# Performance work log

Hardware: AMD Instinct MI355X
Metric: run time of the kernel (lower is better)

## Reference

```python
import jax, jax.numpy as jnp
import numpy as np

CHUNK = 2048   # chunk_size from __init__
EPS = 1e-5     # BatchNorm eps (torch default)


def _proj(x, w, gamma, beta, mean, var):
    # 1x1 conv (no bias) + BatchNorm (eval, running stats) + ReLU
    y = jnp.einsum('bchw,oc->bohw', x, w)
    scale = gamma / jnp.sqrt(var + EPS)
    y = (y - mean[None, :, None, None]) * scale[None, :, None, None] + beta[None, :, None, None]
    return jax.nn.relu(y)


def setup_inputs() -> dict:
    key = jax.random.key(0)
    ks = jax.random.split(key, 8)
    B, Cl, Ci, Co, H, W = 2, 256, 512, 128, 128, 128
    return {
        'lidar_features': jax.random.normal(ks[0], (B, Cl, H, W), jnp.float32),
        'image_features': jax.random.normal(ks[1], (B, Ci, H, W), jnp.float32),
        # kaiming_normal fan_out for 1x1 conv: std = sqrt(2 / Co)
        'lidar_w': jax.random.normal(ks[2], (Co, Cl), jnp.float32) * np.sqrt(2.0 / Co),
        'lidar_gamma': jnp.ones((Co,), jnp.float32),
        'lidar_beta': jnp.zeros((Co,), jnp.float32),
        'lidar_mean': jax.random.normal(ks[3], (Co,), jnp.float32) * 0.1,
        'lidar_var': jax.random.uniform(ks[4], (Co,), jnp.float32, 0.5, 1.5),
        'image_w': jax.random.normal(ks[5], (Co, Ci), jnp.float32) * np.sqrt(2.0 / Co),
        'image_gamma': jnp.ones((Co,), jnp.float32),
        'image_beta': jnp.zeros((Co,), jnp.float32),
        'image_mean': jax.random.normal(ks[6], (Co,), jnp.float32) * 0.1,
        'image_var': jax.random.uniform(ks[7], (Co,), jnp.float32, 0.5, 1.5),
        'modality_weights': jnp.ones((2,), jnp.float32),
    }


def reference(lidar_features, image_features,
              lidar_w, lidar_gamma, lidar_beta, lidar_mean, lidar_var,
              image_w, image_gamma, image_beta, image_mean, image_var,
              modality_weights):
    lidar_proj = _proj(lidar_features, lidar_w, lidar_gamma, lidar_beta, lidar_mean, lidar_var)
    image_proj = _proj(image_features, image_w, image_gamma, image_beta, image_mean, image_var)
    # spatial sizes match by construction, so no interpolation branch
    B, C, H, W = lidar_proj.shape
    P = H * W
    n = P // CHUNK  # P chosen divisible by CHUNK
    # block-diagonal attention: q from image, k=v from lidar, per pixel chunk
    q = image_proj.reshape(B, C, P).transpose(0, 2, 1).reshape(B, n, CHUNK, C)
    k = lidar_proj.reshape(B, C, P).transpose(0, 2, 1).reshape(B, n, CHUNK, C)
    attn = jax.nn.softmax(jnp.einsum('bnqc,bnkc->bnqk', q, k) / jnp.sqrt(jnp.float32(C)), axis=-1)
    out = jnp.einsum('bnqk,bnkc->bnqc', attn, k)  # v == k (both are lidar_proj)
    fused = out.reshape(B, P, C).transpose(0, 2, 1).reshape(B, C, H, W)
    w = jax.nn.softmax(modality_weights)
    return w[0] * image_proj + w[1] * fused
```

## Files before the change

### kernel.cpp

```cpp
#include <hip/hip_runtime.h>
#include <hip/hip_bf16.h>

typedef __attribute__((ext_vector_type(4))) float f32x4;
typedef __attribute__((ext_vector_type(8))) short short8;

#define P_TOT 16384
#define NCO 128
#define EPS 1e-5f
#define ALPHA 0.12752269f

__device__ __forceinline__ unsigned short f2bf(float f) {
  union { float f; unsigned u; } v; v.f = f;
  unsigned r = v.u + 0x7FFFu + ((v.u >> 16) & 1u);
  return (unsigned short)(r >> 16);
}
__device__ __forceinline__ float bf2f(unsigned short h) {
  union { unsigned u; float f; } v; v.u = ((unsigned)h) << 16;
  return v.f;
}
__device__ __forceinline__ unsigned cvtpk_bf16(float lo, float hi) {
  unsigned r;
  asm("v_cvt_pk_bf16_f32 %0, %1, %2" : "=v"(r) : "v"(lo), "v"(hi));
  return r;
}
__device__ __forceinline__ void gload16(const void* g, void* l) {
  __builtin_amdgcn_global_load_lds(
      (const __attribute__((address_space(1))) unsigned*)g,
      (__attribute__((address_space(3))) unsigned*)l, 16, 0, 0);
}

__global__ __launch_bounds__(256) void proj_mfma(
    const float* __restrict__ Xl, const float* __restrict__ Xi,
    const float* __restrict__ Wl, const float* __restrict__ Wi,
    const float* __restrict__ lgm, const float* __restrict__ lbt,
    const float* __restrict__ lmn, const float* __restrict__ lvr,
    const float* __restrict__ igm, const float* __restrict__ ibt,
    const float* __restrict__ imn, const float* __restrict__ ivr,
    unsigned short* __restrict__ Lp, unsigned short* __restrict__ Ip,
    unsigned short* __restrict__ Vg)
{
  __shared__ __align__(16) char smem[36352];
  float* sc_l = (float*)(smem + 35328);
  float* sh_l = (float*)(smem + 35840);

  const int t = threadIdx.x;
  const int w = t >> 6, l = t & 63, l15 = l & 15, g = l >> 4;
  const int zz = blockIdx.y, b = zz & 1, mod = zz >> 1;
  const int pb = blockIdx.x * 128;

  const float* Xg = mod ? Xi : Xl;
  const float* Wg = mod ? Wi : Wl;
  const int Cin = mod ? 512 : 256;
  unsigned short* outp = mod ? Ip : Lp;

  if (t < 128) {
    const float* G = mod ? igm : lgm;
    const float* Bt = mod ? ibt : lbt;
    const float* M = mod ? imn : lmn;
    const float* V = mod ? ivr : lvr;
    float s = G[t] / sqrtf(V[t] + EPS);
    sc_l[t] = s;
    sh_l[t] = Bt[t] - M[t] * s;
  }

  f32x4 o[2][8];
#pragma unroll
  for (int qt = 0; qt < 2; ++qt)
#pragma unroll
    for (int nt = 0; nt < 8; ++nt) o[qt][nt] = (f32x4){0.f, 0.f, 0.f, 0.f};

  uint2 xr[8], wr[8];
  auto load_tiles = [&](int s) {
    int cc = s * 64;
#pragma unroll
    for (int i = 0; i < 8; ++i) {
      int e = t + 256 * i;
      int c = e >> 5, p4 = e & 31;
      f32x4 x = *(const f32x4*)(Xg + ((size_t)(b * Cin + cc + c)) * P_TOT + pb + p4 * 4);
      xr[i].x = cvtpk_bf16(x[0], x[1]);
      xr[i].y = cvtpk_bf16(x[2], x[3]);
    }
#pragma unroll
    for (int i = 0; i < 8; ++i) {
      int e = t + 256 * i;
      int co = e >> 4, c4 = e & 15;
      f32x4 wv = *(const f32x4*)(Wg + (size_t)co * Cin + cc + c4 * 4);
      wr[i].x = cvtpk_bf16(wv[0], wv[1]);
      wr[i].y = cvtpk_bf16(wv[2], wv[3]);
    }
  };

  load_tiles(0);
  const int nsteps = Cin >> 6;
  for (int s = 0; s < nsteps; ++s) {
    __syncthreads();
#pragma unroll
    for (int i = 0; i < 8; ++i) {
      int e = t + 256 * i;
      int c = e >> 5, p4 = e & 31;
      *(uint2*)(smem + c * 264 + p4 * 8) = xr[i];
    }
#pragma unroll
    for (int i = 0; i < 8; ++i) {
      int e = t + 256 * i;
      int co = e >> 4, c4 = e & 15;
      *(uint2*)(smem + 16896 + co * 144 + c4 * 8) = wr[i];
    }
    if (s + 1 < nsteps) load_tiles(s + 1);
    __syncthreads();

#pragma unroll
    for (int kkc = 0; kkc < 2; ++kkc) {
      short8 a[2];
#pragma unroll
      for (int qt = 0; qt < 2; ++qt) {
        const char* ab = smem + (kkc * 32 + g * 8) * 264 + (w * 32 + qt * 16 + l15) * 2;
        union { unsigned uu[4]; short8 v; } cv;
#pragma unroll
        for (int e2 = 0; e2 < 4; ++e2) {
          unsigned lo = *(const unsigned short*)(ab + (2 * e2) * 264);
          unsigned hi = *(const unsigned short*)(ab + (2 * e2 + 1) * 264);
          cv.uu[e2] = lo | (hi << 16);
        }
        a[qt] = cv.v;
      }
#pragma unroll
      for (int nt = 0; nt < 8; ++nt) {
        short8 wf = *(const short8*)(smem + 16896 + (nt * 16 + l15) * 144 + kkc * 64 + g * 16);
        o[0][nt] = __builtin_amdgcn_mfma_f32_16x16x32_bf16(a[0], wf, o[0][nt], 0, 0, 0);
        o[1][nt] = __builtin_amdgcn_mfma_f32_16x16x32_bf16(a[1], wf, o[1][nt], 0, 0, 0);
      }
    }
  }

  __syncthreads();
#pragma unroll
  for (int nt = 0; nt < 8; ++nt) {
    float scv = sc_l[nt * 16 + l15];
    float shv = sh_l[nt * 16 + l15];
#pragma unroll
    for (int qt = 0; qt < 2; ++qt)
#pragma unroll
      for (int r = 0; r < 4; ++r) {
        int p = w * 32 + qt * 16 + 4 * g + r;
        float y = fmaxf(fmaf(o[qt][nt][r], scv, shv), 0.f);
        *(unsigned short*)(smem + p * 272 + (nt * 16 + l15) * 2) = f2bf(y);
      }
  }
  __syncthreads();
  {
    int p = t >> 1, half = t & 1;
    const char* Tb = smem + p * 272 + half * 128;
    unsigned short* ob = outp + ((size_t)b * P_TOT + pb + p) * NCO + half * 64;
#pragma unroll
    for (int i = 0; i < 8; ++i)
      *(uint4*)(ob + i * 8) = *(const uint4*)(Tb + i * 16);
  }
  if (mod == 0) {
    int co = t & 127, ph = t >> 7;
    unsigned short* vb = Vg + ((size_t)b * NCO + co) * P_TOT + pb + ph * 64;
    unsigned pkv[32];
#pragma unroll
    for (int j2 = 0; j2 < 32; ++j2) {
      unsigned lo = *(const unsigned short*)(smem + (ph * 64 + 2 * j2) * 272 + co * 2);
      unsigned hi = *(const unsigned short*)(smem + (ph * 64 + 2 * j2 + 1) * 272 + co * 2);
      pkv[j2] = lo | (hi << 16);
    }
#pragma unroll
    for (int i = 0; i < 8; ++i)
      *(uint4*)(vb + i * 8) = *(const uint4*)&pkv[i * 4];
  }
}

__global__ __launch_bounds__(512) void attn_kernel(
    const unsigned short* __restrict__ Lp,
    const unsigned short* __restrict__ Ip,
    const unsigned short* __restrict__ Vg,
    const float* __restrict__ mw,
    float* __restrict__ out)
{
  __shared__ __align__(16) char smem[131072];

  const int t = threadIdx.x;
  const int half = t >> 8;
  const int t2 = t & 255;
  const int w = t2 >> 6, l = t & 63;
  const int l15 = l & 15, g = l >> 4;
  const int hb = half << 16;
  const int gid = blockIdx.x;
  const int bx = gid >> 4;
  const int chunk = gid & 7;
  const int b = (gid >> 3) & 1;
  const int pq0 = chunk * 2048 + bx * 128;
  const int qw = pq0 + w * 32;

  short8 qf[2][4];
#pragma unroll
  for (int qt = 0; qt < 2; ++qt)
#pragma unroll
    for (int kkc = 0; kkc < 4; ++kkc)
      qf[qt][kkc] = *(const short8*)(Ip +
          ((size_t)b * P_TOT + qw + qt * 16 + l15) * NCO + kkc * 32 + g * 8);

  const char* srcK[4];
  const char* srcV[4];
  int ldsOff[4];
#pragma unroll
  for (int i = 0; i < 4; ++i) {
    int pos = (w * 4 + i) * 4 + (l >> 4);
    int nt = pos >> 4, gp = (pos >> 2) & 3, rr = pos & 3;
    int kp = (nt >> 1) * 32 + gp * 8 + (nt & 1) * 4 + rr;
    srcK[i] = (const char*)Lp +
              ((size_t)b * P_TOT + chunk * 2048 + half * 1024 + kp) * 256 +
              (((l & 15) * 16) ^ ((pos & 7) << 4));
    int c = (w * 4 + i) * 8 + (l >> 3);
    srcV[i] = (const char*)Vg +
              (((size_t)(b * NCO + c)) * P_TOT + chunk * 2048 + half * 1024) * 2 +
              (((l & 7) * 16) ^ ((c & 7) << 4));
    ldsOff[i] = hb + (w * 4 + i) * 1024;
  }

  float m_[2] = {-1e30f, -1e30f}, lsum[2] = {0.f, 0.f};
  f32x4 o[2][8];
#pragma unroll
  for (int qt = 0; qt < 2; ++qt)
#pragma unroll
    for (int ct = 0; ct < 8; ++ct) o[qt][ct] = (f32x4){0.f, 0.f, 0.f, 0.f};

#pragma unroll
  for (int i = 0; i < 4; ++i) {
    gload16(srcK[i], smem + ldsOff[i]);
    gload16(srcV[i], smem + 32768 + ldsOff[i]);
  }
#pragma unroll
  for (int i = 0; i < 4; ++i) {
    gload16(srcK[i] + 16384, smem + 16384 + ldsOff[i]);
    gload16(srcV[i] + 128, smem + 32768 + 16384 + ldsOff[i]);
  }

  for (int kt = 0; kt < 16; ++kt) {
    const int cur = kt & 1;
    if (kt < 15)
      asm volatile("s_waitcnt vmcnt(8)" ::: "memory");
    else
      asm volatile("s_waitcnt vmcnt(0)" ::: "memory");
    __builtin_amdgcn_s_barrier();
    __builtin_amdgcn_sched_barrier(0);

    const char* Kb = smem + hb + cur * 16384;
    const char* Vb = smem + hb + 32768 + cur * 16384;

    f32x4 s[2][4];
#pragma unroll
    for (int qt = 0; qt < 2; ++qt)
#pragma unroll
      for (int nt = 0; nt < 4; ++nt) s[qt][nt] = (f32x4){0.f, 0.f, 0.f, 0.f};
#pragma unroll
    for (int kkc = 0; kkc < 4; ++kkc) {
#pragma unroll
      for (int nt = 0; nt < 4; ++nt) {
        short8 kf = *(const short8*)(Kb + (nt * 16 + l15) * 256 +
                        ((kkc * 64 + g * 16) ^ ((l15 & 7) << 4)));
        s[0][nt] = __builtin_amdgcn_mfma_f32_16x16x32_bf16(kf, qf[0][kkc], s[0][nt], 0, 0, 0);
        s[1][nt] = __builtin_amdgcn_mfma_f32_16x16x32_bf16(kf, qf[1][kkc], s[1][nt], 0, 0, 0);
      }
    }

    unsigned pk[2][4][2];
    float f_[2];
    int upd[2];
#pragma unroll
    for (int qt = 0; qt < 2; ++qt) {
      float v0 = fmaxf(fmaxf(s[qt][0][0], s[qt][0][1]), fmaxf(s[qt][0][2], s[qt][0][3]));
      float v1 = fmaxf(fmaxf(s[qt][1][0], s[qt][1][1]), fmaxf(s[qt][1][2], s[qt][1][3]));
      float v2 = fmaxf(fmaxf(s[qt][2][0], s[qt][2][1]), fmaxf(s[qt][2][2], s[qt][2][3]));
      float v3 = fmaxf(fmaxf(s[qt][3][0], s[qt][3][1]), fmaxf(s[qt][3][2], s[qt][3][3]));
      float v = fmaxf(fmaxf(v0, v1), fmaxf(v2, v3));
      v = fmaxf(v, __shfl_xor(v, 16));
      v = fmaxf(v, __shfl_xor(v, 32));
      float pm = v * ALPHA;
      upd[qt] = __any(pm > m_[qt] + 8.f);
      float mn = m_[qt];
      if (upd[qt]) {
        mn = fmaxf(m_[qt], pm);
        f_[qt] = __builtin_amdgcn_exp2f(m_[qt] - mn);
        m_[qt] = mn;
      } else {
        f_[qt] = 1.f;
      }
      float ps = 0.f;
#pragma unroll
      for (int nt = 0; nt < 4; ++nt) {
#pragma unroll
        for (int r = 0; r < 4; ++r) {
          float p = __builtin_amdgcn_exp2f(s[qt][nt][r] * ALPHA - mn);
          s[qt][nt][r] = p;
          ps += p;
        }
        pk[qt][nt][0] = cvtpk_bf16(s[qt][nt][0], s[qt][nt][1]);
        pk[qt][nt][1] = cvtpk_bf16(s[qt][nt][2], s[qt][nt][3]);
      }
      ps += __shfl_xor(ps, 16);
      ps += __shfl_xor(ps, 32);
      lsum[qt] = lsum[qt] * f_[qt] + ps;
    }

#pragma unroll
    for (int qt = 0; qt < 2; ++qt)
      if (upd[qt]) {
#pragma unroll
        for (int r = 0; r < 4; ++r) {
          float fb = __shfl(f_[qt], 20 * g + r);
#pragma unroll
          for (int ct = 0; ct < 8; ++ct) o[qt][ct][r] *= fb;
        }
      }

#pragma unroll
    for (int kk2 = 0; kk2 < 2; ++kk2) {
      short8 af[2];
#pragma unroll
      for (int qt = 0; qt < 2; ++qt) {
        union { unsigned u[4]; short8 v; } x;
        x.u[0] = pk[qt][2 * kk2][0];
        x.u[1] = pk[qt][2 * kk2][1];
        x.u[2] = pk[qt][2 * kk2 + 1][0];
        x.u[3] = pk[qt][2 * kk2 + 1][1];
        af[qt] = x.v;
      }
#pragma unroll
      for (int ct = 0; ct < 8; ++ct) {
        short8 vf = *(const short8*)(Vb + (ct * 16 + l15) * 128 +
                        ((kk2 * 64 + g * 16) ^ ((l15 & 7) << 4)));
        o[0][ct] = __builtin_amdgcn_mfma_f32_16x16x32_bf16(af[0], vf, o[0][ct], 0, 0, 0);
        o[1][ct] = __builtin_amdgcn_mfma_f32_16x16x32_bf16(af[1], vf, o[1][ct], 0, 0, 0);
      }
    }

    __builtin_amdgcn_s_barrier();
    __builtin_amdgcn_sched_barrier(0);
    if (kt + 2 < 16) {
#pragma unroll
      for (int i = 0; i < 4; ++i) {
        gload16(srcK[i] + (size_t)(kt + 2) * 16384,
                smem + cur * 16384 + ldsOff[i]);
        gload16(srcV[i] + (size_t)(kt + 2) * 128,
                smem + 32768 + cur * 16384 + ldsOff[i]);
      }
    }
  }

  float* Tp = (float*)smem;
  float* m1a = (float*)(smem + 67584);
  float* l1a = (float*)(smem + 68096);

  if (half == 1) {
#pragma unroll
    for (int qt = 0; qt < 2; ++qt) {
      int qb = w * 32 + qt * 16 + 4 * g;
#pragma unroll
      for (int ct = 0; ct < 8; ++ct) {
        int c = ct * 16 + l15;
        *(f32x4*)&Tp[c * 132 + qb] = o[qt][ct];
      }
      if (g == 0) {
        m1a[w * 32 + qt * 16 + l15] = m_[qt];
        l1a[w * 32 + qt * 16 + l15] = lsum[qt];
      }
    }
  }
  __syncthreads();

  float a0 = mw[0], a1 = mw[1];
  float mx = fmaxf(a0, a1);
  float e0 = __builtin_amdgcn_exp2f((a0 - mx) * 1.442695041f);
  float e1 = __builtin_amdgcn_exp2f((a1 - mx) * 1.442695041f);
  float w0m = e0 / (e0 + e1), w1m = e1 / (e0 + e1);

  if (half == 0) {
#pragma unroll
    for (int qt = 0; qt < 2; ++qt) {
      int qb = w * 32 + qt * 16 + 4 * g;
      f32x4 m1v = *(const f32x4*)&m1a[qb];
      f32x4 l1v = *(const f32x4*)&l1a[qb];
      float A[4], Bc[4];
#pragma unroll
      for (int r = 0; r < 4; ++r) {
        float m0r = __shfl(m_[qt], 20 * g + r);
        float l0r = __shfl(lsum[qt], 20 * g + r);
        float M = fmaxf(m0r, m1v[r]);
        float w0h = __builtin_amdgcn_exp2f(m0r - M);
        float w1h = __builtin_amdgcn_exp2f(m1v[r] - M);
        float L = w0h * l0r + w1h * l1v[r];
        A[r] = w1m * w0h / L;
        Bc[r] = w1m * w1h / L;
      }
#pragma unroll
      for (int ct = 0; ct < 8; ++ct) {
        int c = ct * 16 + l15;
        f32x4 o1 = *(const f32x4*)&Tp[c * 132 + qb];
#pragma unroll
        for (int r = 0; r < 4; ++r)
          o[qt][ct][r] = A[r] * o[qt][ct][r] + Bc[r] * o1[r];
      }
    }
  }
  __syncthreads();

  if (half == 0) {
#pragma unroll
    for (int qt = 0; qt < 2; ++qt) {
      int qb = w * 32 + qt * 16 + 4 * g;
#pragma unroll
      for (int ct = 0; ct < 8; ++ct) {
        int c = ct * 16 + l15;
        f32x4 v = o[qt][ct];
#pragma unroll
        for (int r = 0; r < 4; ++r) {
          float img = bf2f(Ip[((size_t)b * P_TOT + pq0 + qb + r) * NCO + c]);
          v[r] = w0m * img + v[r];
        }
        *(f32x4*)&Tp[c * 132 + qb] = v;
      }
    }
  }
  __syncthreads();
  {
    int cc = t >> 5;
    int q0 = (t & 31) * 4;
#pragma unroll
    for (int i2 = 0; i2 < 8; ++i2) {
      int c = cc + i2 * 16;
      float* Ob = out + ((size_t)b * NCO + c) * P_TOT + pq0 + q0;
      *(f32x4*)Ob = *(const f32x4*)&Tp[c * 132 + q0];
    }
  }
}

extern "C" void kernel_launch(void* const* d_in, const int* in_sizes, int n_in,
                              void* d_out, int out_size, void* d_ws, size_t ws_size,
                              hipStream_t stream) {
  const float* lidar = (const float*)d_in[0];
  const float* image = (const float*)d_in[1];
  const float* lw = (const float*)d_in[2];
  const float* lg = (const float*)d_in[3];
  const float* lb = (const float*)d_in[4];
  const float* lm = (const float*)d_in[5];
  const float* lv = (const float*)d_in[6];
  const float* iw = (const float*)d_in[7];
  const float* ig = (const float*)d_in[8];
  const float* ibt = (const float*)d_in[9];
  const float* im = (const float*)d_in[10];
  const float* iv = (const float*)d_in[11];
  const float* mw = (const float*)d_in[12];

  unsigned short* Lp = (unsigned short*)d_ws;
  unsigned short* Ip = Lp + (size_t)2 * P_TOT * NCO;
  unsigned short* Vg = Ip + (size_t)2 * P_TOT * NCO;

  dim3 gp(P_TOT / 128, 4);
  proj_mfma<<<gp, 256, 0, stream>>>(lidar, image, lw, iw,
                                    lg, lb, lm, lv, ig, ibt, im, iv,
                                    Lp, Ip, Vg);

  attn_kernel<<<dim3(256), 512, 0, stream>>>(Lp, Ip, Vg, mw, (float*)d_out);
}
```

Measured before the change: 84.83 us.

## Software-pipeline QK^T of next tile with softmax/PV of current tile

Restructures the attention main loop so the QK^T MFMAs for tile kt+1 are issued before the softmax and PV work of tile kt, using two ping-pong score register sets. K and V staging are split so K for tile kt+2 is loaded right after the next QK^T, and V is loaded only after the current PV finishes. The goal is to overlap exp/softmax VALU work with MFMA work and loosen the wait counts. It costs extra registers for a second score buffer, which may lower occupancy.

Result: slower. 89.21 us (+5.2%).

```diff
diff --git a/kernel.cpp b/kernel.cpp
--- a/kernel.cpp
+++ b/kernel.cpp
@@ -227,30 +227,18 @@
 #pragma unroll
     for (int ct = 0; ct < 8; ++ct) o[qt][ct] = (f32x4){0.f, 0.f, 0.f, 0.f};
 
-#pragma unroll
-  for (int i = 0; i < 4; ++i) {
-    gload16(srcK[i], smem + ldsOff[i]);
-    gload16(srcV[i], smem + 32768 + ldsOff[i]);
-  }
-#pragma unroll
-  for (int i = 0; i < 4; ++i) {
-    gload16(srcK[i] + 16384, smem + 16384 + ldsOff[i]);
-    gload16(srcV[i] + 128, smem + 32768 + 16384 + ldsOff[i]);
-  }
-
-  for (int kt = 0; kt < 16; ++kt) {
-    const int cur = kt & 1;
-    if (kt < 15)
-      asm volatile("s_waitcnt vmcnt(8)" ::: "memory");
-    else
-      asm volatile("s_waitcnt vmcnt(0)" ::: "memory");
-    __builtin_amdgcn_s_barrier();
-    __builtin_amdgcn_sched_barrier(0);
-
-    const char* Kb = smem + hb + cur * 16384;
-    const char* Vb = smem + hb + 32768 + cur * 16384;
-
-    f32x4 s[2][4];
+  auto stageK = [&](int tile) {
+#pragma unroll
+    for (int i = 0; i < 4; ++i)
+      gload16(srcK[i] + (size_t)tile * 16384, smem + (tile & 1) * 16384 + ldsOff[i]);
+  };
+  auto stageV = [&](int tile) {
+#pragma unroll
+    for (int i = 0; i < 4; ++i)
+      gload16(srcV[i] + (size_t)tile * 128, smem + 32768 + (tile & 1) * 16384 + ldsOff[i]);
+  };
+  auto qkt = [&](int tile, f32x4 (&s)[2][4]) {
+    const char* Kb = smem + hb + (tile & 1) * 16384;
 #pragma unroll
     for (int qt = 0; qt < 2; ++qt)
 #pragma unroll
@@ -265,7 +253,10 @@
         s[1][nt] = __builtin_amdgcn_mfma_f32_16x16x32_bf16(kf, qf[1][kkc], s[1][nt], 0, 0, 0);
       }
     }
-
+  };
+
+  auto finish = [&](int tile, f32x4 (&s)[2][4]) {
+    const char* Vb = smem + hb + 32768 + (tile & 1) * 16384;
     unsigned pk[2][4][2];
     float f_[2];
     int upd[2];
@@ -304,7 +295,6 @@
       ps += __shfl_xor(ps, 32);
       lsum[qt] = lsum[qt] * f_[qt] + ps;
     }
-
 #pragma unroll
     for (int qt = 0; qt < 2; ++qt)
       if (upd[qt]) {
@@ -315,7 +305,6 @@
           for (int ct = 0; ct < 8; ++ct) o[qt][ct][r] *= fb;
         }
       }
-
 #pragma unroll
     for (int kk2 = 0; kk2 < 2; ++kk2) {
       short8 af[2];
@@ -336,18 +325,38 @@
         o[1][ct] = __builtin_amdgcn_mfma_f32_16x16x32_bf16(af[1], vf, o[1][ct], 0, 0, 0);
       }
     }
-
+  };
+
+  f32x4 sA[2][4], sB[2][4];
+
+  stageK(0); stageV(0); stageK(1); stageV(1);
+  asm volatile("s_waitcnt vmcnt(4)" ::: "memory");
+  __builtin_amdgcn_s_barrier();
+  __builtin_amdgcn_sched_barrier(0);
+  qkt(0, sA);
+
+  auto step = [&](int kt, f32x4 (&scur)[2][4], f32x4 (&snxt)[2][4]) {
+    if (kt < 15) {
+      asm volatile("s_waitcnt vmcnt(4)" ::: "memory");
+      __builtin_amdgcn_s_barrier();
+      __builtin_amdgcn_sched_barrier(0);
+      qkt(kt + 1, snxt);
+      if (kt + 2 < 16) stageK(kt + 2);
+    } else {
+      asm volatile("s_waitcnt vmcnt(0)" ::: "memory");
+      __builtin_amdgcn_s_barrier();
+      __builtin_amdgcn_sched_barrier(0);
+    }
+    finish(kt, scur);
     __builtin_amdgcn_s_barrier();
     __builtin_amdgcn_sched_barrier(0);
-    if (kt + 2 < 16) {
-#pragma unroll
-      for (int i = 0; i < 4; ++i) {
-        gload16(srcK[i] + (size_t)(kt + 2) * 16384,
-                smem + cur * 16384 + ldsOff[i]);
-        gload16(srcV[i] + (size_t)(kt + 2) * 128,
-                smem + 32768 + cur * 16384 + ldsOff[i]);
-      }
-    }
+    if (kt + 2 < 16) stageV(kt + 2);
+  };
+
+#pragma unroll 1
+  for (int kt2 = 0; kt2 < 8; ++kt2) {
+    step(2 * kt2, sA, sB);
+    step(2 * kt2 + 1, sB, sA);
   }
 
   float* Tp = (float*)smem;
```
